# Kernel optimization log

Measured on AMD Instinct MI355X. Metric: run time of the kernel, lower is better.

Reference implementation:

```python
import jax, jax.numpy as jnp
import numpy as np

N, D, H, DK, DEG = 8192, 512, 8, 64, 16
E = N * DEG
M = N


def setup_inputs() -> dict:
    key = jax.random.key(0)
    ks = jax.random.split(key, 12)
    x = jax.random.normal(ks[0], (N, D), dtype=jnp.float32)
    # every node has DEG neighbors -> sorted row index, random cols
    row_index = jnp.repeat(jnp.arange(N, dtype=jnp.int64), DEG)
    col_index = jax.random.randint(ks[1], (E,), 0, M, dtype=jnp.int64)
    to_col_index = jax.random.randint(ks[2], (M,), 0, N, dtype=jnp.int64)
    att_bias = 0.1 * jax.random.normal(ks[3], (H, E), dtype=jnp.float32)
    pos = 10.0 * jax.random.uniform(ks[4], (N, 3), dtype=jnp.float32)
    col_pos = 10.0 * jax.random.uniform(ks[5], (M, 3), dtype=jnp.float32)
    dist = jnp.linalg.norm(col_pos[col_index] - pos[row_index], axis=-1)
    s = 1.0 / np.sqrt(D)
    Wq = s * jax.random.normal(ks[6], (H, DK, D), dtype=jnp.float32)
    Wqv = s * jax.random.normal(ks[7], (H, 3, D), dtype=jnp.float32)
    Wk = s * jax.random.normal(ks[8], (H, DK, D), dtype=jnp.float32)
    Wv = s * jax.random.normal(ks[9], (H, DK, D), dtype=jnp.float32)
    Wout = s * jax.random.normal(ks[10], (D, D + 4 * H), dtype=jnp.float32)
    bout = jnp.zeros((D,), dtype=jnp.float32)
    return {"x": x, "row_index": row_index, "col_index": col_index,
            "to_col_index": to_col_index, "att_bias": att_bias, "dist": dist,
            "pos": pos, "col_pos": col_pos, "Wq": Wq, "Wqv": Wqv, "Wk": Wk,
            "Wv": Wv, "Wout": Wout, "bout": bout}


def reference(x, row_index, col_index, to_col_index, att_bias, dist, pos,
              col_pos, Wq, Wqv, Wk, Wv, Wout, bout):
    n = x.shape[0]
    dk = Wq.shape[1]
    scale = 1.0 / jnp.sqrt(jnp.asarray(dk, x.dtype))
    # per-head projections: [H, N, dk]
    q = jnp.einsum('nd,hkd->hnk', x, Wq) * scale
    qv = jnp.einsum('nd,hkd->hnk', x, Wqv)              # [H, N, 3]
    kx = jnp.einsum('nd,hkd->hnk', x, Wk)[:, to_col_index]  # [H, M, dk]
    vx = jnp.einsum('nd,hkd->hnk', x, Wv)[:, to_col_index]
    # gather per edge -> [E, H, *]
    qe = q[:, row_index].transpose(1, 0, 2)
    ke = kx[:, col_index].transpose(1, 0, 2)
    qve = qv[:, row_index].transpose(1, 0, 2)           # [E, H, 3]
    rel = col_pos[col_index] - pos[row_index]           # [E, 3]
    dist_e = jnp.where(dist == 0, jnp.inf, dist)        # masked_fill(dist==0, inf)
    # angular = qv_row . col_pos_col - qv_row . pos_row = qv_row . rel
    angular = jnp.einsum('ehc,ec->eh', qve, rel)
    logit = jnp.einsum('ehk,ehk->eh', qe, ke) + att_bias.T + angular / dist_e[:, None]
    # sparse (per-row segment) softmax
    m = jax.ops.segment_max(logit, row_index, num_segments=n)
    p = jnp.exp(logit - m[row_index])
    s = jax.ops.segment_sum(p, row_index, num_segments=n)
    att = p / s[row_index]                              # [E, H]
    natt = att / dist_e[:, None]
    dst_vec = jax.ops.segment_sum(natt[:, :, None] * col_pos[col_index][:, None, :],
                                  row_index, num_segments=n)   # [N, H, 3]
    avg_inv_dist = jax.ops.segment_sum(natt, row_index, num_segments=n)  # [N, H]
    src_vec = avg_inv_dist[:, :, None] * pos[:, None, :]
    diff = dst_vec - src_vec
    feat3 = diff / jnp.maximum(jnp.linalg.norm(diff, axis=-1, keepdims=True), 1e-12)
    ve = vx[:, col_index].transpose(1, 0, 2)            # [E, H, dk]
    y = jax.ops.segment_sum(att[:, :, None] * ve, row_index, num_segments=n)  # [N, H, dk]
    feat = jnp.concatenate([y, feat3, avg_inv_dist[:, :, None]], axis=-1)
    feat = feat.reshape(n, -1)                          # [N, H*(dk+4)]
    return feat @ Wout.T + bout
```

## Files before the change

### kernel.cpp

```cpp
#include <hip/hip_runtime.h>
#include <math.h>

#define N_NODES 8192
#define D_FEAT  512
#define H_HEADS 8
#define DKH     64
#define DEG     16
#define E_EDGES (N_NODES * DEG)
#define FEAT_W  544
#define OUT_W   512
#define QKV_W   1664

typedef unsigned short u16;
typedef __attribute__((ext_vector_type(8))) short short8;
typedef __attribute__((ext_vector_type(8))) unsigned short us8;
typedef __attribute__((ext_vector_type(4))) float f32x4;

__device__ __forceinline__ u16 f2bf(float f) {
    union { float f; unsigned u; } c; c.f = f;
    unsigned u = c.u;
    unsigned r = u + 0x7FFFu + ((u >> 16) & 1u);
    return (u16)(r >> 16);
}
__device__ __forceinline__ float bf2f(u16 h) {
    union { unsigned u; float f; } c; c.u = ((unsigned)h) << 16;
    return c.f;
}

__device__ __forceinline__ void async16(const void* g, void* l) {
#if __has_builtin(__builtin_amdgcn_global_load_lds)
    __builtin_amdgcn_global_load_lds(
        (const __attribute__((address_space(1))) void*)g,
        (__attribute__((address_space(3))) void*)l, 16, 0, 0);
#else
    *(float4*)l = *(const float4*)g;
#endif
}

template<bool HAS_BL, bool BF16_OUT>
__global__ __launch_bounds__(256) void gemm_mfma(
    const u16* __restrict__ Ah,
    const u16* __restrict__ Bh, const u16* __restrict__ Bl,
    const float* __restrict__ bias, void* __restrict__ Cout,
    int M, int N, int K)
{
    constexpr int NB = HAS_BL ? 2 : 1;
    __shared__ u16 smem[128 * 32 * (1 + NB)];
    u16* sAh = smem;
    u16* sBh = smem + 128 * 32;
    u16* sBl = smem + 128 * 32 * 2;

    const int tid  = threadIdx.x;
    const int bm   = blockIdx.y * 128;
    const int bn   = blockIdx.x * 128;
    const int wave = tid >> 6;
    const int lane = tid & 63;
    const int wr   = (wave >> 1) * 64;
    const int wc   = (wave & 1) * 64;
    const int lrow = lane & 15;
    const int quad = lane >> 4;

    f32x4 acc[4][4];
    #pragma unroll
    for (int i = 0; i < 4; ++i)
        #pragma unroll
        for (int j = 0; j < 4; ++j) {
            f32x4 z = {0.f, 0.f, 0.f, 0.f};
            acc[i][j] = z;
        }

    for (int k0 = 0; k0 < K; k0 += 32) {
        #pragma unroll
        for (int i = 0; i < 2; ++i) {
            const int lin = i * 256 + tid;
            const int row = lin >> 2;
            const int seg = (lin & 3) << 3;
            const int loff = lin << 3;
            const size_t ga = (size_t)(bm + row) * K + k0 + seg;
            const size_t gb = (size_t)(bn + row) * K + k0 + seg;
            async16(Ah + ga, sAh + loff);
            async16(Bh + gb, sBh + loff);
            if (HAS_BL) async16(Bl + gb, sBl + loff);
        }
        __syncthreads();

        short8 a_h[4], b_h[4], b_l[4];
        #pragma unroll
        for (int t = 0; t < 4; ++t) {
            const int ar = (wr + t * 16 + lrow) * 32 + quad * 8;
            const int br = (wc + t * 16 + lrow) * 32 + quad * 8;
            a_h[t] = *(const short8*)&sAh[ar];
            b_h[t] = *(const short8*)&sBh[br];
            if (HAS_BL) b_l[t] = *(const short8*)&sBl[br];
        }

        #pragma unroll
        for (int mt = 0; mt < 4; ++mt)
            #pragma unroll
            for (int nt = 0; nt < 4; ++nt) {
                acc[mt][nt] = __builtin_amdgcn_mfma_f32_16x16x32_bf16(
                    a_h[mt], b_h[nt], acc[mt][nt], 0, 0, 0);
                if (HAS_BL)
                    acc[mt][nt] = __builtin_amdgcn_mfma_f32_16x16x32_bf16(
                        a_h[mt], b_l[nt], acc[mt][nt], 0, 0, 0);
            }
        __syncthreads();
    }

    #pragma unroll
    for (int nt = 0; nt < 4; ++nt) {
        const int col = bn + wc + nt * 16 + lrow;
        const float bb = bias ? bias[col] : 0.f;
        #pragma unroll
        for (int mt = 0; mt < 4; ++mt) {
            #pragma unroll
            for (int r = 0; r < 4; ++r) {
                const int row = bm + wr + mt * 16 + quad * 4 + r;
                const float v = acc[mt][nt][r] + bb;
                if (BF16_OUT)
                    ((u16*)Cout)[(size_t)row * N + col] = f2bf(v);
                else
                    ((float*)Cout)[(size_t)row * N + col] = v;
            }
        }
    }
}

__global__ __launch_bounds__(256) void cvt_bf16(
    const float* __restrict__ in, u16* __restrict__ out, int n4, float scale)
{
    const int i = blockIdx.x * 256 + threadIdx.x;
    if (i >= n4) return;
    float4 v = ((const float4*)in)[i];
    ushort4 h;
    h.x = f2bf(v.x * scale); h.y = f2bf(v.y * scale);
    h.z = f2bf(v.z * scale); h.w = f2bf(v.w * scale);
    ((ushort4*)out)[i] = h;
}

__global__ __launch_bounds__(256) void split2(
    const float* __restrict__ in, u16* __restrict__ hi, u16* __restrict__ lo, int n4)
{
    const int i = blockIdx.x * 256 + threadIdx.x;
    if (i >= n4) return;
    const float4 v = ((const float4*)in)[i];
    ushort4 h, l;
    h.x = f2bf(v.x); l.x = f2bf(v.x - bf2f(h.x));
    h.y = f2bf(v.y); l.y = f2bf(v.y - bf2f(h.y));
    h.z = f2bf(v.z); l.z = f2bf(v.z - bf2f(h.z));
    h.w = f2bf(v.w); l.w = f2bf(v.w - bf2f(h.w));
    ((ushort4*)hi)[i] = h;
    ((ushort4*)lo)[i] = l;
}

__global__ __launch_bounds__(256) void build_B(
    const float* __restrict__ Wq, const float* __restrict__ Wk,
    const float* __restrict__ Wv, const float* __restrict__ Wqv,
    u16* __restrict__ B)
{
    const int idx = blockIdx.x * 256 + threadIdx.x;
    if (idx >= QKV_W * (D_FEAT / 4)) return;
    const int row = idx >> 7;
    const int c4  = idx & 127;
    float4 v = make_float4(0.f, 0.f, 0.f, 0.f);
    float scale = 1.f;
    if (row < 512) {
        v = *(const float4*)(Wq + (size_t)row * 512 + c4 * 4);
        scale = 0.125f;
    } else if (row < 1024) {
        v = *(const float4*)(Wk + (size_t)(row - 512) * 512 + c4 * 4);
    } else if (row < 1536) {
        v = *(const float4*)(Wv + (size_t)(row - 1024) * 512 + c4 * 4);
    } else if (row < 1560) {
        v = *(const float4*)(Wqv + (size_t)(row - 1536) * 512 + c4 * 4);
    }
    ushort4 h;
    h.x = f2bf(v.x * scale); h.y = f2bf(v.y * scale);
    h.z = f2bf(v.z * scale); h.w = f2bf(v.w * scale);
    ((ushort4*)B)[idx] = h;
}

__global__ __launch_bounds__(256) void edge_kernel(
    const u16* __restrict__ qkv,
    const int* __restrict__ col_index, const int* __restrict__ to_col,
    const float* __restrict__ att_bias, const float* __restrict__ dist,
    const float* __restrict__ pos, const float* __restrict__ col_pos,
    u16* __restrict__ feat)
{
    const int wave = threadIdx.x >> 6;
    const int lane = threadIdx.x & 63;
    const int n = blockIdx.x * 4 + wave;
    const int h = lane >> 3;
    const int sub = lane & 7;

    const size_t qbase = (size_t)n * QKV_W;

    float qf[8];
    {
        const us8 qu = *(const us8*)(qkv + qbase + h * DKH + sub * 8);
        #pragma unroll
        for (int i = 0; i < 8; ++i) qf[i] = bf2f(qu[i]);
    }
    float qv0, qv1, qv2;
    {
        const float qvl = bf2f(qkv[qbase + 1536 + (lane < 24 ? lane : 0)]);
        qv0 = __shfl(qvl, h * 3 + 0);
        qv1 = __shfl(qvl, h * 3 + 1);
        qv2 = __shfl(qvl, h * 3 + 2);
    }
    const float px = pos[3 * n + 0], py = pos[3 * n + 1], pz = pos[3 * n + 2];

    const int j16 = lane & 15;
    const int e0  = n * DEG + j16;
    const int c_l  = col_index[e0];
    const int cc_l = to_col[c_l];
    const float d_l = dist[e0];
    const float invd_l = (d_l == 0.f) ? 0.f : (1.f / d_l);
    const float rx_l = col_pos[3 * c_l + 0] - px;
    const float ry_l = col_pos[3 * c_l + 1] - py;
    const float rz_l = col_pos[3 * c_l + 2] - pz;

    const float b0 = att_bias[(size_t)h * E_EDGES + n * DEG + sub * 2 + 0];
    const float b1 = att_bias[(size_t)h * E_EDGES + n * DEG + sub * 2 + 1];

    float logit[DEG];
    #pragma unroll
    for (int j = 0; j < DEG; ++j) {
        const int cc = __shfl(cc_l, j);
        const us8 ku = *(const us8*)(qkv + (size_t)cc * QKV_W + 512 + h * DKH + sub * 8);
        float dot = 0.f;
        #pragma unroll
        for (int i = 0; i < 8; ++i) dot += qf[i] * bf2f(ku[i]);
        dot += __shfl_xor(dot, 1, 8);
        dot += __shfl_xor(dot, 2, 8);
        dot += __shfl_xor(dot, 4, 8);
        const float invd = __shfl(invd_l, j);
        const float ang = qv0 * __shfl(rx_l, j) + qv1 * __shfl(ry_l, j)
                        + qv2 * __shfl(rz_l, j);
        const float bj = __shfl((j & 1) ? b1 : b0, j >> 1, 8);
        logit[j] = dot + bj + ang * invd;
    }

    float m = logit[0];
    #pragma unroll
    for (int j = 1; j < DEG; ++j) m = fmaxf(m, logit[j]);
    float s = 0.f;
    #pragma unroll
    for (int j = 0; j < DEG; ++j) { logit[j] = __expf(logit[j] - m); s += logit[j]; }
    const float inv_s = 1.f / s;

    float y[8] = {0.f, 0.f, 0.f, 0.f, 0.f, 0.f, 0.f, 0.f};
    float dx = 0.f, dy = 0.f, dz = 0.f, aid = 0.f;
    #pragma unroll
    for (int j = 0; j < DEG; ++j) {
        const float a = logit[j] * inv_s;
        const int cc = __shfl(cc_l, j);
        const us8 vu = *(const us8*)(qkv + (size_t)cc * QKV_W + 1024 + h * DKH + sub * 8);
        #pragma unroll
        for (int i = 0; i < 8; ++i) y[i] += a * bf2f(vu[i]);
        const float na = a * __shfl(invd_l, j);
        dx += na * __shfl(rx_l, j);
        dy += na * __shfl(ry_l, j);
        dz += na * __shfl(rz_l, j);
        aid += na;
    }

    u16* f = feat + (size_t)n * FEAT_W + h * (DKH + 4);
    ushort4 o0, o1;
    o0.x = f2bf(y[0]); o0.y = f2bf(y[1]); o0.z = f2bf(y[2]); o0.w = f2bf(y[3]);
    o1.x = f2bf(y[4]); o1.y = f2bf(y[5]); o1.z = f2bf(y[6]); o1.w = f2bf(y[7]);
    *(ushort4*)(f + sub * 8 + 0) = o0;
    *(ushort4*)(f + sub * 8 + 4) = o1;
    if (sub == 0) {
        const float nrm = sqrtf(dx * dx + dy * dy + dz * dz);
        const float rn = 1.f / fmaxf(nrm, 1e-12f);
        ushort4 ex;
        ex.x = f2bf(dx * rn); ex.y = f2bf(dy * rn);
        ex.z = f2bf(dz * rn); ex.w = f2bf(aid);
        *(ushort4*)(f + DKH) = ex;
    }
}

extern "C" void kernel_launch(void* const* d_in, const int* in_sizes, int n_in,
                              void* d_out, int out_size, void* d_ws, size_t ws_size,
                              hipStream_t stream)
{
    const float* x         = (const float*)d_in[0];
    const int*   col_index = (const int*)d_in[2];
    const int*   to_col    = (const int*)d_in[3];
    const float* att_bias  = (const float*)d_in[4];
    const float* dist      = (const float*)d_in[5];
    const float* pos       = (const float*)d_in[6];
    const float* col_pos   = (const float*)d_in[7];
    const float* Wq        = (const float*)d_in[8];
    const float* Wqv       = (const float*)d_in[9];
    const float* Wk        = (const float*)d_in[10];
    const float* Wv        = (const float*)d_in[11];
    const float* Wout      = (const float*)d_in[12];
    const float* bout      = (const float*)d_in[13];
    float* out = (float*)d_out;

    char* ws = (char*)d_ws;
    u16* qkv   = (u16*)(ws + 0);
    u16* xh    = (u16*)(ws + 27262976);
    u16* Bfuse = (u16*)(ws + 35651584);
    u16* Woth  = (u16*)(ws + 37355520);
    u16* Wotl  = (u16*)(ws + 37912576);
    u16* feat  = (u16*)(ws + 38469632);

    dim3 blk(256);

    hipLaunchKernelGGL(cvt_bf16, dim3(N_NODES * D_FEAT / 4 / 256), blk, 0, stream,
                       x, xh, N_NODES * D_FEAT / 4, 1.0f);
    hipLaunchKernelGGL(build_B, dim3((QKV_W * (D_FEAT / 4) + 255) / 256), blk, 0, stream,
                       Wq, Wk, Wv, Wqv, Bfuse);
    hipLaunchKernelGGL(split2, dim3((OUT_W * FEAT_W / 4 + 255) / 256), blk, 0, stream,
                       Wout, Woth, Wotl, OUT_W * FEAT_W / 4);

    hipLaunchKernelGGL((gemm_mfma<false, true>), dim3(QKV_W / 128, N_NODES / 128),
                       blk, 0, stream,
                       xh, Bfuse, (const u16*)nullptr, (const float*)nullptr,
                       (void*)qkv, N_NODES, QKV_W, D_FEAT);

    hipLaunchKernelGGL(edge_kernel, dim3(N_NODES / 4), blk, 0, stream,
                       qkv, col_index, to_col, att_bias, dist, pos, col_pos, feat);

    hipLaunchKernelGGL((gemm_mfma<true, false>), dim3(OUT_W / 128, N_NODES / 128),
                       blk, 0, stream,
                       feat, Woth, Wotl, bout, (void*)out,
                       N_NODES, OUT_W, FEAT_W);
}
```

Baseline: 188.6 us.

## Merge prep kernels into one launch and use online softmax in edge kernel

Replaces the three separate conversion kernels (x to bf16, fused QKV weight build, Wout hi/lo split) with a single block-range-dispatched prep kernel, which removes two launches. The edge kernel becomes a single-pass online softmax: K and V rows for each neighbor are loaded together, and the y, direction and inverse-distance accumulators are rescaled as the running max changes. This drops the second gather pass and the logit array. In exchange it adds two exps per edge and the rescale multiplies.

```diff
diff --git a/kernel.cpp b/kernel.cpp
--- a/kernel.cpp
+++ b/kernel.cpp
@@ -126,58 +126,54 @@
     }
 }
 
-__global__ __launch_bounds__(256) void cvt_bf16(
-    const float* __restrict__ in, u16* __restrict__ out, int n4, float scale)
-{
-    const int i = blockIdx.x * 256 + threadIdx.x;
-    if (i >= n4) return;
-    float4 v = ((const float4*)in)[i];
-    ushort4 h;
-    h.x = f2bf(v.x * scale); h.y = f2bf(v.y * scale);
-    h.z = f2bf(v.z * scale); h.w = f2bf(v.w * scale);
-    ((ushort4*)out)[i] = h;
-}
-
-__global__ __launch_bounds__(256) void split2(
-    const float* __restrict__ in, u16* __restrict__ hi, u16* __restrict__ lo, int n4)
-{
-    const int i = blockIdx.x * 256 + threadIdx.x;
-    if (i >= n4) return;
-    const float4 v = ((const float4*)in)[i];
-    ushort4 h, l;
-    h.x = f2bf(v.x); l.x = f2bf(v.x - bf2f(h.x));
-    h.y = f2bf(v.y); l.y = f2bf(v.y - bf2f(h.y));
-    h.z = f2bf(v.z); l.z = f2bf(v.z - bf2f(h.z));
-    h.w = f2bf(v.w); l.w = f2bf(v.w - bf2f(h.w));
-    ((ushort4*)hi)[i] = h;
-    ((ushort4*)lo)[i] = l;
-}
-
-__global__ __launch_bounds__(256) void build_B(
+__global__ __launch_bounds__(256) void prep_kernel(
+    const float* __restrict__ x,
     const float* __restrict__ Wq, const float* __restrict__ Wk,
     const float* __restrict__ Wv, const float* __restrict__ Wqv,
-    u16* __restrict__ B)
+    const float* __restrict__ Wout,
+    u16* __restrict__ xh, u16* __restrict__ B,
+    u16* __restrict__ Woth, u16* __restrict__ Wotl)
 {
-    const int idx = blockIdx.x * 256 + threadIdx.x;
-    if (idx >= QKV_W * (D_FEAT / 4)) return;
-    const int row = idx >> 7;
-    const int c4  = idx & 127;
-    float4 v = make_float4(0.f, 0.f, 0.f, 0.f);
-    float scale = 1.f;
-    if (row < 512) {
-        v = *(const float4*)(Wq + (size_t)row * 512 + c4 * 4);
-        scale = 0.125f;
-    } else if (row < 1024) {
-        v = *(const float4*)(Wk + (size_t)(row - 512) * 512 + c4 * 4);
-    } else if (row < 1536) {
-        v = *(const float4*)(Wv + (size_t)(row - 1024) * 512 + c4 * 4);
-    } else if (row < 1560) {
-        v = *(const float4*)(Wqv + (size_t)(row - 1536) * 512 + c4 * 4);
-    }
-    ushort4 h;
-    h.x = f2bf(v.x * scale); h.y = f2bf(v.y * scale);
-    h.z = f2bf(v.z * scale); h.w = f2bf(v.w * scale);
-    ((ushort4*)B)[idx] = h;
+    const int b = blockIdx.x;
+    const int tid = threadIdx.x;
+    if (b < 4096) {
+        const int i = b * 256 + tid;
+        const float4 v = ((const float4*)x)[i];
+        ushort4 h;
+        h.x = f2bf(v.x); h.y = f2bf(v.y); h.z = f2bf(v.z); h.w = f2bf(v.w);
+        ((ushort4*)xh)[i] = h;
+    } else if (b < 4928) {
+        const int idx = (b - 4096) * 256 + tid;
+        const int row = idx >> 7;
+        const int c4  = idx & 127;
+        float4 v = make_float4(0.f, 0.f, 0.f, 0.f);
+        float scale = 1.f;
+        if (row < 512) {
+            v = *(const float4*)(Wq + (size_t)row * 512 + c4 * 4);
+            scale = 0.125f;
+        } else if (row < 1024) {
+            v = *(const float4*)(Wk + (size_t)(row - 512) * 512 + c4 * 4);
+        } else if (row < 1536) {
+            v = *(const float4*)(Wv + (size_t)(row - 1024) * 512 + c4 * 4);
+        } else if (row < 1560) {
+            v = *(const float4*)(Wqv + (size_t)(row - 1536) * 512 + c4 * 4);
+        }
+        ushort4 h;
+        h.x = f2bf(v.x * scale); h.y = f2bf(v.y * scale);
+        h.z = f2bf(v.z * scale); h.w = f2bf(v.w * scale);
+        ((ushort4*)B)[idx] = h;
+    } else {
+        const int i = (b - 4928) * 256 + tid;
+        if (i >= OUT_W * FEAT_W / 4) return;
+        const float4 v = ((const float4*)Wout)[i];
+        ushort4 h, l;
+        h.x = f2bf(v.x); l.x = f2bf(v.x - bf2f(h.x));
+        h.y = f2bf(v.y); l.y = f2bf(v.y - bf2f(h.y));
+        h.z = f2bf(v.z); l.z = f2bf(v.z - bf2f(h.z));
+        h.w = f2bf(v.w); l.w = f2bf(v.w - bf2f(h.w));
+        ((ushort4*)Woth)[i] = h;
+        ((ushort4*)Wotl)[i] = l;
+    }
 }
 
 __global__ __launch_bounds__(256) void edge_kernel(
@@ -194,10 +190,11 @@
     const int sub = lane & 7;
 
     const size_t qbase = (size_t)n * QKV_W;
+    const int hoff = h * DKH + sub * 8;
 
     float qf[8];
     {
-        const us8 qu = *(const us8*)(qkv + qbase + h * DKH + sub * 8);
+        const us8 qu = *(const us8*)(qkv + qbase + hoff);
         #pragma unroll
         for (int i = 0; i < 8; ++i) qf[i] = bf2f(qu[i]);
     }
@@ -223,11 +220,16 @@
     const float b0 = att_bias[(size_t)h * E_EDGES + n * DEG + sub * 2 + 0];
     const float b1 = att_bias[(size_t)h * E_EDGES + n * DEG + sub * 2 + 1];
 
-    float logit[DEG];
+    float m = -3.0e38f, s = 0.f;
+    float y[8] = {0.f, 0.f, 0.f, 0.f, 0.f, 0.f, 0.f, 0.f};
+    float dx = 0.f, dy = 0.f, dz = 0.f, aid = 0.f;
+
     #pragma unroll
     for (int j = 0; j < DEG; ++j) {
         const int cc = __shfl(cc_l, j);
-        const us8 ku = *(const us8*)(qkv + (size_t)cc * QKV_W + 512 + h * DKH + sub * 8);
+        const u16* rowp = qkv + (size_t)cc * QKV_W + hoff;
+        const us8 ku = *(const us8*)(rowp + 512);
+        const us8 vu = *(const us8*)(rowp + 1024);
         float dot = 0.f;
         #pragma unroll
         for (int i = 0; i < 8; ++i) dot += qf[i] * bf2f(ku[i]);
@@ -235,40 +237,35 @@
         dot += __shfl_xor(dot, 2, 8);
         dot += __shfl_xor(dot, 4, 8);
         const float invd = __shfl(invd_l, j);
-        const float ang = qv0 * __shfl(rx_l, j) + qv1 * __shfl(ry_l, j)
-                        + qv2 * __shfl(rz_l, j);
+        const float rx = __shfl(rx_l, j);
+        const float ry = __shfl(ry_l, j);
+        const float rz = __shfl(rz_l, j);
+        const float ang = qv0 * rx + qv1 * ry + qv2 * rz;
         const float bj = __shfl((j & 1) ? b1 : b0, j >> 1, 8);
-        logit[j] = dot + bj + ang * invd;
-    }
-
-    float m = logit[0];
-    #pragma unroll
-    for (int j = 1; j < DEG; ++j) m = fmaxf(m, logit[j]);
-    float s = 0.f;
-    #pragma unroll
-    for (int j = 0; j < DEG; ++j) { logit[j] = __expf(logit[j] - m); s += logit[j]; }
+        const float l = dot + bj + ang * invd;
+
+        const float mn   = fmaxf(m, l);
+        const float corr = __expf(m - mn);
+        const float p    = __expf(l - mn);
+        s = s * corr + p;
+        #pragma unroll
+        for (int i = 0; i < 8; ++i) y[i] = y[i] * corr + p * bf2f(vu[i]);
+        const float pn = p * invd;
+        dx = dx * corr + pn * rx;
+        dy = dy * corr + pn * ry;
+        dz = dz * corr + pn * rz;
+        aid = aid * corr + pn;
+        m = mn;
+    }
     const float inv_s = 1.f / s;
-
-    float y[8] = {0.f, 0.f, 0.f, 0.f, 0.f, 0.f, 0.f, 0.f};
-    float dx = 0.f, dy = 0.f, dz = 0.f, aid = 0.f;
-    #pragma unroll
-    for (int j = 0; j < DEG; ++j) {
-        const float a = logit[j] * inv_s;
-        const int cc = __shfl(cc_l, j);
-        const us8 vu = *(const us8*)(qkv + (size_t)cc * QKV_W + 1024 + h * DKH + sub * 8);
-        #pragma unroll
-        for (int i = 0; i < 8; ++i) y[i] += a * bf2f(vu[i]);
-        const float na = a * __shfl(invd_l, j);
-        dx += na * __shfl(rx_l, j);
-        dy += na * __shfl(ry_l, j);
-        dz += na * __shfl(rz_l, j);
-        aid += na;
-    }
+    dx *= inv_s; dy *= inv_s; dz *= inv_s; aid *= inv_s;
 
     u16* f = feat + (size_t)n * FEAT_W + h * (DKH + 4);
     ushort4 o0, o1;
-    o0.x = f2bf(y[0]); o0.y = f2bf(y[1]); o0.z = f2bf(y[2]); o0.w = f2bf(y[3]);
-    o1.x = f2bf(y[4]); o1.y = f2bf(y[5]); o1.z = f2bf(y[6]); o1.w = f2bf(y[7]);
+    o0.x = f2bf(y[0] * inv_s); o0.y = f2bf(y[1] * inv_s);
+    o0.z = f2bf(y[2] * inv_s); o0.w = f2bf(y[3] * inv_s);
+    o1.x = f2bf(y[4] * inv_s); o1.y = f2bf(y[5] * inv_s);
+    o1.z = f2bf(y[6] * inv_s); o1.w = f2bf(y[7] * inv_s);
     *(ushort4*)(f + sub * 8 + 0) = o0;
     *(ushort4*)(f + sub * 8 + 4) = o1;
     if (sub == 0) {
@@ -310,12 +307,8 @@
 
     dim3 blk(256);
 
-    hipLaunchKernelGGL(cvt_bf16, dim3(N_NODES * D_FEAT / 4 / 256), blk, 0, stream,
-                       x, xh, N_NODES * D_FEAT / 4, 1.0f);
-    hipLaunchKernelGGL(build_B, dim3((QKV_W * (D_FEAT / 4) + 255) / 256), blk, 0, stream,
-                       Wq, Wk, Wv, Wqv, Bfuse);
-    hipLaunchKernelGGL(split2, dim3((OUT_W * FEAT_W / 4 + 255) / 256), blk, 0, stream,
-                       Wout, Woth, Wotl, OUT_W * FEAT_W / 4);
+    hipLaunchKernelGGL(prep_kernel, dim3(5200), blk, 0, stream,
+                       x, Wq, Wk, Wv, Wqv, Wout, xh, Bfuse, Woth, Wotl);
 
     hipLaunchKernelGGL((gemm_mfma<false, true>), dim3(QKV_W / 128, N_NODES / 128),
                        blk, 0, stream,
```

Result: slower. 210.9 us (+11.8%).
